# Performance work log

Hardware: AMD Instinct MI355X
Metric: run time of the kernel (lower is better)

Reference implementation:

```python
import jax, jax.numpy as jnp
import numpy as np

B, C, H, W = 4, 256, 64, 64
CK = C // 8   # 32, theta/phi channels
CV = C // 2   # 128, g channels


def setup_inputs() -> dict:
    key = jax.random.key(0)
    ks = jax.random.split(key, 10)
    s = lambda fan: 1.0 / np.sqrt(fan)
    inp = {
        "x": jax.random.normal(ks[0], (B, C, H, W), dtype=jnp.float32),
        "theta_w": jax.random.normal(ks[1], (CK, C), dtype=jnp.float32) * s(C),
        "theta_b": jax.random.normal(ks[2], (CK,), dtype=jnp.float32) * 0.01,
        "phi_w": jax.random.normal(ks[3], (CK, C), dtype=jnp.float32) * s(C),
        "phi_b": jax.random.normal(ks[4], (CK,), dtype=jnp.float32) * 0.01,
        "g_w": jax.random.normal(ks[5], (CV, C), dtype=jnp.float32) * s(C),
        "g_b": jax.random.normal(ks[6], (CV,), dtype=jnp.float32) * 0.01,
        "o_w": jax.random.normal(ks[7], (C, CV), dtype=jnp.float32) * s(CV),
        "o_b": jax.random.normal(ks[8], (C,), dtype=jnp.float32) * 0.01,
        "gamma": jax.random.normal(ks[9], (1,), dtype=jnp.float32) * 0.1,
    }
    return inp


def reference(x, theta_w, theta_b, phi_w, phi_b, g_w, g_b, o_w, o_b, gamma):
    b, c, h, w = x.shape
    n = h * w
    xf = x.reshape(b, c, n)  # [B, C, N]
    # 1x1 convs == per-pixel linear projections
    theta = jnp.einsum('oc,bcn->bon', theta_w, xf) + theta_b[None, :, None]  # [B, CK, N]
    phi = jnp.einsum('oc,bcn->bon', phi_w, xf) + phi_b[None, :, None]        # [B, CK, N]
    g = jnp.einsum('oc,bcn->bon', g_w, xf) + g_b[None, :, None]              # [B, CV, N]
    # scores[b, i, j] = theta_i . phi_j ; softmax over dim=1 (query axis i) as in torch code
    scores = jnp.einsum('bci,bcj->bij', theta, phi)  # [B, N, N]
    attention = jax.nn.softmax(scores, axis=1)
    # o_pre = bmm(g, attention^T): o_pre[b, c, i] = sum_j g[b, c, j] * attention[b, i, j]
    o_pre = jnp.einsum('bcj,bij->bci', g, attention)  # [B, CV, N]
    o = jnp.einsum('oc,bcn->bon', o_w, o_pre) + o_b[None, :, None]  # [B, C, N]
    out = (gamma[0] * o + xf).reshape(b, c, h, w)
    return out
```

## Files before the change

kernel.cpp:

```cpp
#include <hip/hip_runtime.h>
#include <math.h>

#define B_  4
#define C_  256
#define N_  4096
#define CK_ 32
#define CV_ 128

typedef __attribute__((ext_vector_type(8))) short short8;
typedef __attribute__((ext_vector_type(4))) float f32x4;
typedef unsigned short u16;
typedef unsigned int   u32;

static constexpr float LOG2E = 1.4426950408889634f;

static __device__ __forceinline__ u16 f2bf(float f) {
    u32 u = __float_as_uint(f);
    u = (u + 0x7FFFu + ((u >> 16) & 1u)) >> 16;
    return (u16)u;
}
static __device__ __forceinline__ float bf2f(u16 h) {
    return __uint_as_float(((u32)h) << 16);
}

static __device__ __forceinline__ float fexp2(float x) {
#if __has_builtin(__builtin_amdgcn_exp2f)
    return __builtin_amdgcn_exp2f(x);
#else
    float r; asm("v_exp_f32 %0, %1\n\ts_nop 0" : "=v"(r) : "v"(x)); return r;
#endif
}
static __device__ __forceinline__ float frcp(float x) {
#if __has_builtin(__builtin_amdgcn_rcpf)
    return __builtin_amdgcn_rcpf(x);
#else
    float r; asm("v_rcp_f32 %0, %1\n\ts_nop 0" : "=v"(r) : "v"(x)); return r;
#endif
}
static __device__ __forceinline__ u32 cvt_pk_bf16(float a, float b) {
    u32 r; asm("v_cvt_pk_bf16_f32 %0, %1, %2" : "=v"(r) : "v"(a), "v"(b));
    return r;
}

__global__ __launch_bounds__(256) void prep_kernel(
    const float* __restrict__ x, u16* __restrict__ xT16,
    const float* __restrict__ theta_w, const float* __restrict__ phi_w,
    const float* __restrict__ g_w,     const float* __restrict__ o_w,
    u16* __restrict__ W16, u16* __restrict__ ow16)
{
    if (blockIdx.x >= N_ / 64) {
        const int base = (((blockIdx.x - N_ / 64) * 16 + blockIdx.y * 4 + blockIdx.z) * 256
                          + threadIdx.x) * 4;
        #pragma unroll
        for (int e0 = 0; e0 < 4; ++e0) {
            const int e = base + e0;
            if (e < 8192)        W16[e] = f2bf(theta_w[e] * LOG2E);
            else if (e < 16384)  W16[e] = f2bf(phi_w[e - 8192]);
            else if (e < 49152)  W16[e] = f2bf(g_w[e - 16384]);
            else                 ow16[e - 49152] = f2bf(o_w[e - 49152]);
        }
        return;
    }

    const int b = blockIdx.z, c0 = blockIdx.y * 64, n0 = blockIdx.x * 64;
    const int t = threadIdx.x;
    __shared__ float tile[64][65];

    const int cr = t >> 4, nc = (t & 15) * 4;
    #pragma unroll
    for (int it = 0; it < 4; ++it) {
        const float4 v = *(const float4*)(x + (size_t)(b * C_ + c0 + cr + it * 16) * N_ + n0 + nc);
        tile[cr + it * 16][nc + 0] = v.x; tile[cr + it * 16][nc + 1] = v.y;
        tile[cr + it * 16][nc + 2] = v.z; tile[cr + it * 16][nc + 3] = v.w;
    }
    __syncthreads();
    const int n = t >> 2, cg = (t & 3) * 16;
    union { u16 us[16]; uint4 u4[2]; } pk;
    #pragma unroll
    for (int e = 0; e < 16; ++e) pk.us[e] = f2bf(tile[cg + e][n]);
    uint4* dst = (uint4*)(xT16 + (size_t)(b * N_ + n0 + n) * C_ + c0 + cg);
    dst[0] = pk.u4[0]; dst[1] = pk.u4[1];
}

__global__ __launch_bounds__(256) void proj_mfma_kernel(
    const u16* __restrict__ xT16, const u16* __restrict__ W16,
    const float* __restrict__ theta_b, const float* __restrict__ phi_b,
    const float* __restrict__ g_b,
    u16* __restrict__ theta_t, u16* __restrict__ phi_t, u16* __restrict__ g2)
{
    const int b = blockIdx.y, n0 = blockIdx.x * 64;
    const int w = threadIdx.x >> 6, lane = threadIdx.x & 63;
    const int lr = lane & 15, q = lane >> 4;
    const f32x4 zf = {0.f, 0.f, 0.f, 0.f};

    const u16* xrow = xT16 + (size_t)(b * N_ + n0 + w * 16 + lr) * C_;
    f32x4 acc[4];
    #pragma unroll
    for (int nt = 0; nt < 4; ++nt) acc[nt] = zf;
    for (int ks = 0; ks < 8; ++ks) {
        const short8 aX = *(const short8*)(xrow + ks * 32 + q * 8);
        #pragma unroll
        for (int nt = 0; nt < 4; ++nt) {
            const short8 bW = *(const short8*)(W16 + (size_t)(nt * 16 + lr) * C_ + ks * 32 + q * 8);
            acc[nt] = __builtin_amdgcn_mfma_f32_16x16x32_bf16(aX, bW, acc[nt], 0, 0, 0);
        }
    }
    #pragma unroll
    for (int nt = 0; nt < 4; ++nt) {
        const int o = nt * 16 + lr;
        #pragma unroll
        for (int reg = 0; reg < 4; ++reg) {
            const int n = n0 + w * 16 + q * 4 + reg;
            if (nt < 2)
                theta_t[(size_t)(b * N_ + n) * CK_ + o] = f2bf(acc[nt][reg] + theta_b[o] * LOG2E);
            else
                phi_t[(size_t)(b * N_ + n) * CK_ + (o - 32)] = f2bf(acc[nt][reg] + phi_b[o - 32]);
        }
    }

    #pragma unroll
    for (int mp = 0; mp < 2; ++mp) {
        const int ctile = w * 2 + mp;
        const int crow = ctile * 16;
        f32x4 ag[4];
        #pragma unroll
        for (int nt = 0; nt < 4; ++nt) ag[nt] = zf;
        for (int ks = 0; ks < 8; ++ks) {
            const short8 aW = *(const short8*)(W16 + (size_t)(64 + crow + lr) * C_ + ks * 32 + q * 8);
            #pragma unroll
            for (int nt = 0; nt < 4; ++nt) {
                const short8 bX = *(const short8*)(xT16 + (size_t)(b * N_ + n0 + nt * 16 + lr) * C_ + ks * 32 + q * 8);
                ag[nt] = __builtin_amdgcn_mfma_f32_16x16x32_bf16(aW, bX, ag[nt], 0, 0, 0);
            }
        }
        #pragma unroll
        for (int nt = 0; nt < 4; ++nt) {
            const int jchunk = (n0 >> 5) + (nt >> 1);
            const int lhi = (nt & 1) * 2 + (lr >> 3);
            #pragma unroll
            for (int reg = 0; reg < 4; ++reg) {
                const int c = crow + q * 4 + reg;
                const int lane2 = (q * 4 + reg) + 16 * lhi;
                g2[((size_t)(b * 8 + ctile) * 128 + jchunk) * 512 + lane2 * 8 + (lr & 7)]
                    = f2bf(ag[nt][reg] + g_b[c]);
            }
        }
    }
}

__global__ __launch_bounds__(256) void colstats_kernel(
    const u16* __restrict__ theta_t, const u16* __restrict__ phi_t,
    float* __restrict__ Z)
{
    const int b  = blockIdx.z;
    const int j0 = blockIdx.x * 32;
    const int istart = blockIdx.y * (N_ / 4);
    const int tid = threadIdx.x;
    const int wave = tid >> 6, lane = tid & 63;
    const int lr = lane & 15, q = lane >> 4;

    const int jW = j0 + (wave & 1) * 16;
    const short8 bF = *(const short8*)(phi_t + (size_t)(b * N_ + jW + lr) * CK_ + q * 8);

    const u16* thp = theta_t + (size_t)b * N_ * CK_;
    const f32x4 zero = {0.f, 0.f, 0.f, 0.f};
    float zacc = 0.f;
    for (int it = istart + (wave >> 1) * 16; it < istart + N_ / 4; it += 32) {
        const short8 aF = *(const short8*)(thp + (size_t)(it + lr) * CK_ + q * 8);
        f32x4 S = __builtin_amdgcn_mfma_f32_16x16x32_bf16(aF, bF, zero, 0, 0, 0);
        zacc += fexp2(S[0]) + fexp2(S[1]) + fexp2(S[2]) + fexp2(S[3]);
    }
    zacc += __shfl_xor(zacc, 16);
    zacc += __shfl_xor(zacc, 32);
    if (lane < 16) atomicAdd(&Z[(size_t)b * N_ + jW + lr], zacc);
}

__global__ __launch_bounds__(256) void gscale_kernel(
    u16* __restrict__ g2, const float* __restrict__ Z)
{
    const size_t idx = ((size_t)blockIdx.x * 256 + threadIdx.x) * 8;
    const int b = (int)(idx >> 19);
    const int j = (int)(((idx >> 9) & 127) * 32 + ((idx >> 7) & 3) * 8);
    uint4 raw = *(const uint4*)(g2 + idx);
    const float4 z0 = *(const float4*)(Z + (size_t)b * N_ + j);
    const float4 z1 = *(const float4*)(Z + (size_t)b * N_ + j + 4);
    const float zz[8] = {z0.x, z0.y, z0.z, z0.w, z1.x, z1.y, z1.z, z1.w};
    u16* pr = (u16*)&raw;
    union { u16 us[8]; uint4 u4; } pk;
    #pragma unroll
    for (int k = 0; k < 8; ++k) pk.us[k] = f2bf(bf2f(pr[k]) * frcp(zz[k]));
    *(uint4*)(g2 + idx) = pk.u4;
}

__global__ __launch_bounds__(256, 1) void opre_kernel(
    const u16* __restrict__ theta_t, const u16* __restrict__ phi_t,
    const u16* __restrict__ g2,
    float* __restrict__ o_p0, float* __restrict__ o_p1, u16* __restrict__ opb)
{
    const int bx = blockIdx.x;
    const int igg = bx & 7, ch = (bx >> 3) & 3, jq = (bx >> 5) & 3, b = bx >> 7;
    const int w = threadIdx.x >> 6, lane = threadIdx.x & 63;
    const int lr = lane & 15, q = lane >> 4;
    const int i0 = (igg * 4 + w) * 128;
    const f32x4 zf = {0.f, 0.f, 0.f, 0.f};

    short8 bT[8];
    #pragma unroll
    for (int it = 0; it < 8; ++it)
        bT[it] = *(const short8*)(theta_t + (size_t)(b * N_ + i0 + it * 16 + lr) * CK_ + q * 8);

    const int ja = (lr >> 2) * 8 + (lr & 3);
    const int jstart = jq * (N_ / 4);
    const u16* pA = phi_t + ((size_t)(b * N_) + jstart + ja) * CK_ + q * 8;
    const u16* pG = g2 + ((size_t)(b * 8 + ch * 2) * 128 + jq * 32) * 512 + lane * 8;

    f32x4 acc[8][2];
    #pragma unroll
    for (int it = 0; it < 8; ++it) { acc[it][0] = zf; acc[it][1] = zf; }

    short8 A0a = *(const short8*)(pA);
    short8 A1a = *(const short8*)(pA + 4 * CK_);
    short8 G0a = *(const short8*)(pG);
    short8 G1a = *(const short8*)(pG + 128 * 512);
    short8 A0b = *(const short8*)(pA + 32 * CK_);
    short8 A1b = *(const short8*)(pA + 36 * CK_);
    short8 G0b = *(const short8*)(pG + 512);
    short8 G1b = *(const short8*)(pG + 128 * 512 + 512);

#define OPRE_CHUNK(K, A0r, A1r, G0r, G1r)                                          \
    {                                                                               \
        const short8 cA0 = A0r, cA1 = A1r, cG0 = G0r, cG1 = G1r;                    \
        const int kn = ((K) + 2) & 31;                                              \
        A0r = *(const short8*)(pA + (size_t)kn * (32 * CK_));                       \
        A1r = *(const short8*)(pA + (size_t)kn * (32 * CK_) + 4 * CK_);             \
        G0r = *(const short8*)(pG + kn * 512);                                      \
        G1r = *(const short8*)(pG + 128 * 512 + kn * 512);                          \
        _Pragma("unroll")                                                           \
        for (int it = 0; it < 8; ++it) {                                            \
            const f32x4 Sa = __builtin_amdgcn_mfma_f32_16x16x32_bf16(cA0, bT[it], zf, 0, 0, 0); \
            const f32x4 Sb = __builtin_amdgcn_mfma_f32_16x16x32_bf16(cA1, bT[it], zf, 0, 0, 0); \
            union { u32 u[4]; short8 s8; } ef;                                      \
            ef.u[0] = cvt_pk_bf16(fexp2(Sa[0]), fexp2(Sa[1]));                      \
            ef.u[1] = cvt_pk_bf16(fexp2(Sa[2]), fexp2(Sa[3]));                      \
            ef.u[2] = cvt_pk_bf16(fexp2(Sb[0]), fexp2(Sb[1]));                      \
            ef.u[3] = cvt_pk_bf16(fexp2(Sb[2]), fexp2(Sb[3]));                      \
            acc[it][0] = __builtin_amdgcn_mfma_f32_16x16x32_bf16(ef.s8, cG0, acc[it][0], 0, 0, 0); \
            acc[it][1] = __builtin_amdgcn_mfma_f32_16x16x32_bf16(ef.s8, cG1, acc[it][1], 0, 0, 0); \
        }                                                                           \
    }

    for (int k = 0; k < 32; k += 2) {
        OPRE_CHUNK(k,     A0a, A1a, G0a, G1a)
        OPRE_CHUNK(k + 1, A0b, A1b, G0b, G1b)
    }
#undef OPRE_CHUNK

    if (jq < 2) {
        float* op = (jq ? o_p1 : o_p0);
        #pragma unroll
        for (int it = 0; it < 8; ++it) {
            const size_t tb = ((size_t)(b * 256 + (i0 >> 4) + it) * 4 + ch) * 512;
            #pragma unroll
            for (int ct = 0; ct < 2; ++ct) {
                #pragma unroll
                for (int reg = 0; reg < 4; ++reg) {
                    const int lane2 = (q * 4 + reg) + 16 * (ct * 2 + (lr >> 3));
                    op[tb + lane2 * 8 + (lr & 7)] = acc[it][ct][reg];
                }
            }
        }
    } else {
        u16* ob = opb + (size_t)(jq - 2) * ((size_t)B_ * N_ * CV_);
        #pragma unroll
        for (int it = 0; it < 8; ++it) {
            const size_t tb = ((size_t)(b * 256 + (i0 >> 4) + it) * 4 + ch) * 512;
            #pragma unroll
            for (int ct = 0; ct < 2; ++ct) {
                #pragma unroll
                for (int reg = 0; reg < 4; ++reg) {
                    const int lane2 = (q * 4 + reg) + 16 * (ct * 2 + (lr >> 3));
                    ob[tb + lane2 * 8 + (lr & 7)] = f2bf(acc[it][ct][reg]);
                }
            }
        }
    }
}

__global__ __launch_bounds__(256) void final_mfma_kernel(
    const float* __restrict__ o_p0, const float* __restrict__ o_p1,
    const u16* __restrict__ opb,
    const u16* __restrict__ ow16, const float* __restrict__ o_b,
    const float* __restrict__ gamma, const float* __restrict__ x,
    float* __restrict__ out)
{
    const int b = blockIdx.y, n0 = blockIdx.x * 32;
    const int w = threadIdx.x >> 6, lane = threadIdx.x & 63;
    const int lr = lane & 15, q = lane >> 4;
    const f32x4 zf = {0.f, 0.f, 0.f, 0.f};
    const size_t QS = (size_t)B_ * N_ * CV_;

    f32x4 acc[4][2];
    #pragma unroll
    for (int mt = 0; mt < 4; ++mt)
        #pragma unroll
        for (int nt = 0; nt < 2; ++nt) acc[mt][nt] = zf;

    for (int ks = 0; ks < 4; ++ks) {
        short8 bP[2];
        #pragma unroll
        for (int nt = 0; nt < 2; ++nt) {
            const size_t base = (((size_t)(b * 256 + (n0 >> 4) + nt) * 4 + ks) * 64 + lane) * 8;
            const float4 a0 = *(const float4*)(o_p0 + base);
            const float4 a1 = *(const float4*)(o_p0 + base + 4);
            const float4 c0 = *(const float4*)(o_p1 + base);
            const float4 c1 = *(const float4*)(o_p1 + base + 4);
            union { u16 us[8]; uint4 u4; } w2, w3;
            w2.u4 = *(const uint4*)(opb + base);
            w3.u4 = *(const uint4*)(opb + QS + base);
            float s[8] = {a0.x + c0.x, a0.y + c0.y, a0.z + c0.z, a0.w + c0.w,
                          a1.x + c1.x, a1.y + c1.y, a1.z + c1.z, a1.w + c1.w};
            #pragma unroll
            for (int e = 0; e < 8; ++e)
                s[e] += bf2f(w2.us[e]) + bf2f(w3.us[e]);
            union { u32 u[4]; short8 s8; } pk;
            pk.u[0] = cvt_pk_bf16(s[0], s[1]);
            pk.u[1] = cvt_pk_bf16(s[2], s[3]);
            pk.u[2] = cvt_pk_bf16(s[4], s[5]);
            pk.u[3] = cvt_pk_bf16(s[6], s[7]);
            bP[nt] = pk.s8;
        }
        #pragma unroll
        for (int mt = 0; mt < 4; ++mt) {
            const short8 aW = *(const short8*)(ow16 + (size_t)((w * 4 + mt) * 16 + lr) * CV_ + ks * 32 + q * 8);
            #pragma unroll
            for (int nt = 0; nt < 2; ++nt)
                acc[mt][nt] = __builtin_amdgcn_mfma_f32_16x16x32_bf16(aW, bP[nt], acc[mt][nt], 0, 0, 0);
        }
    }

    const float gm = gamma[0];
    #pragma unroll
    for (int mt = 0; mt < 4; ++mt) {
        #pragma unroll
        for (int nt = 0; nt < 2; ++nt) {
            #pragma unroll
            for (int reg = 0; reg < 4; ++reg) {
                const int oc = (w * 4 + mt) * 16 + q * 4 + reg;
                const int n = n0 + nt * 16 + lr;
                const size_t off = (size_t)(b * C_ + oc) * N_ + n;
                out[off] = x[off] + gm * (acc[mt][nt][reg] + o_b[oc]);
            }
        }
    }
}

extern "C" void kernel_launch(void* const* d_in, const int* in_sizes, int n_in,
                              void* d_out, int out_size, void* d_ws, size_t ws_size,
                              hipStream_t stream)
{
    const float* x       = (const float*)d_in[0];
    const float* theta_w = (const float*)d_in[1];
    const float* theta_b = (const float*)d_in[2];
    const float* phi_w   = (const float*)d_in[3];
    const float* phi_b   = (const float*)d_in[4];
    const float* g_w     = (const float*)d_in[5];
    const float* g_b     = (const float*)d_in[6];
    const float* o_w     = (const float*)d_in[7];
    const float* o_b     = (const float*)d_in[8];
    const float* gamma   = (const float*)d_in[9];
    float* out = (float*)d_out;

    u16* xT16    = (u16*)d_ws;
    u16* W16     = xT16 + (size_t)B_ * N_ * C_;
    u16* ow16    = W16 + 192 * C_;
    u16* theta_t = ow16 + C_ * CV_;
    u16* phi_t   = theta_t + (size_t)B_ * N_ * CK_;
    u16* g2      = phi_t + (size_t)B_ * N_ * CK_;
    float* Z     = (float*)(g2 + (size_t)B_ * CV_ * N_);
    float* o_p0  = Z + (size_t)B_ * N_;
    float* o_p1  = o_p0 + (size_t)B_ * N_ * CV_;
    u16* opb     = xT16;

    hipMemsetAsync(Z, 0, (size_t)B_ * N_ * sizeof(float), stream);

    prep_kernel<<<dim3(N_ / 64 + 5, C_ / 64, B_), 256, 0, stream>>>(
        x, xT16, theta_w, phi_w, g_w, o_w, W16, ow16);
    proj_mfma_kernel<<<dim3(N_ / 64, B_), 256, 0, stream>>>(
        xT16, W16, theta_b, phi_b, g_b, theta_t, phi_t, g2);
    colstats_kernel<<<dim3(N_ / 32, 4, B_), 256, 0, stream>>>(theta_t, phi_t, Z);
    gscale_kernel<<<dim3((B_ * CV_ * N_) / 2048), 256, 0, stream>>>(g2, Z);
    opre_kernel<<<dim3(512), 256, 0, stream>>>(theta_t, phi_t, g2, o_p0, o_p1, opb);
    final_mfma_kernel<<<dim3(N_ / 32, B_), 256, 0, stream>>>(
        o_p0, o_p1, opb, ow16, o_b, gamma, x, out);
}
```

Baseline: 193.7 us.

## Share exp-score tiles across channel waves through LDS in opre kernel

Before, each block handled one 32-channel slice of g, and its four waves covered different query rows. Every channel slice therefore recomputed the same theta·phi score MFMAs and exp2 values, four times over. Now a block owns 128 query rows and its four waves split the channels. Each wave computes exp scores for two 16-row tiles and writes them to a double-buffered LDS array, and all waves read all eight tiles for their PV MFMAs. This cuts score MFMAs and transcendental work by a factor of four, at the cost of a __syncthreads per chunk and extra LDS traffic.

```diff
diff --git a/kernel.cpp b/kernel.cpp
--- a/kernel.cpp
+++ b/kernel.cpp
@@ -198,21 +198,21 @@
     float* __restrict__ o_p0, float* __restrict__ o_p1, u16* __restrict__ opb)
 {
     const int bx = blockIdx.x;
-    const int igg = bx & 7, ch = (bx >> 3) & 3, jq = (bx >> 5) & 3, b = bx >> 7;
+    const int igg = bx & 31, jq = (bx >> 5) & 3, b = bx >> 7;
     const int w = threadIdx.x >> 6, lane = threadIdx.x & 63;
     const int lr = lane & 15, q = lane >> 4;
-    const int i0 = (igg * 4 + w) * 128;
+    const int i0 = igg * 128;
     const f32x4 zf = {0.f, 0.f, 0.f, 0.f};
 
-    short8 bT[8];
-    #pragma unroll
-    for (int it = 0; it < 8; ++it)
-        bT[it] = *(const short8*)(theta_t + (size_t)(b * N_ + i0 + it * 16 + lr) * CK_ + q * 8);
+    __shared__ u16 El[2][8 * 512];
+
+    const short8 bT0 = *(const short8*)(theta_t + (size_t)(b * N_ + i0 + (2 * w) * 16 + lr) * CK_ + q * 8);
+    const short8 bT1 = *(const short8*)(theta_t + (size_t)(b * N_ + i0 + (2 * w + 1) * 16 + lr) * CK_ + q * 8);
 
     const int ja = (lr >> 2) * 8 + (lr & 3);
     const int jstart = jq * (N_ / 4);
     const u16* pA = phi_t + ((size_t)(b * N_) + jstart + ja) * CK_ + q * 8;
-    const u16* pG = g2 + ((size_t)(b * 8 + ch * 2) * 128 + jq * 32) * 512 + lane * 8;
+    const u16* pG = g2 + ((size_t)(b * 8 + w * 2) * 128 + jq * 32) * 512 + lane * 8;
 
     f32x4 acc[8][2];
     #pragma unroll
@@ -227,7 +227,11 @@
     short8 G0b = *(const short8*)(pG + 512);
     short8 G1b = *(const short8*)(pG + 128 * 512 + 512);
 
-#define OPRE_CHUNK(K, A0r, A1r, G0r, G1r)                                          \
+    u16* const myE0 = &El[0][(2 * w) * 512 + lane * 8];
+    u16* const myE1 = &El[0][(2 * w + 1) * 512 + lane * 8];
+    const int bufstep = 8 * 512;
+
+#define OPRE_CHUNK(K, BUF, A0r, A1r, G0r, G1r)                                     \
     {                                                                               \
         const short8 cA0 = A0r, cA1 = A1r, cG0 = G0r, cG1 = G1r;                    \
         const int kn = ((K) + 2) & 31;                                              \
@@ -235,23 +239,34 @@
         A1r = *(const short8*)(pA + (size_t)kn * (32 * CK_) + 4 * CK_);             \
         G0r = *(const short8*)(pG + kn * 512);                                      \
         G1r = *(const short8*)(pG + 128 * 512 + kn * 512);                          \
+                                                 \
+        const f32x4 Sa0 = __builtin_amdgcn_mfma_f32_16x16x32_bf16(cA0, bT0, zf, 0, 0, 0); \
+        const f32x4 Sb0 = __builtin_amdgcn_mfma_f32_16x16x32_bf16(cA1, bT0, zf, 0, 0, 0); \
+        const f32x4 Sa1 = __builtin_amdgcn_mfma_f32_16x16x32_bf16(cA0, bT1, zf, 0, 0, 0); \
+        const f32x4 Sb1 = __builtin_amdgcn_mfma_f32_16x16x32_bf16(cA1, bT1, zf, 0, 0, 0); \
+        union { u32 u[4]; short8 s8; } e0, e1;                                      \
+        e0.u[0] = cvt_pk_bf16(fexp2(Sa0[0]), fexp2(Sa0[1]));                        \
+        e0.u[1] = cvt_pk_bf16(fexp2(Sa0[2]), fexp2(Sa0[3]));                        \
+        e0.u[2] = cvt_pk_bf16(fexp2(Sb0[0]), fexp2(Sb0[1]));                        \
+        e0.u[3] = cvt_pk_bf16(fexp2(Sb0[2]), fexp2(Sb0[3]));                        \
+        e1.u[0] = cvt_pk_bf16(fexp2(Sa1[0]), fexp2(Sa1[1]));                        \
+        e1.u[1] = cvt_pk_bf16(fexp2(Sa1[2]), fexp2(Sa1[3]));                        \
+        e1.u[2] = cvt_pk_bf16(fexp2(Sb1[0]), fexp2(Sb1[1]));                        \
+        e1.u[3] = cvt_pk_bf16(fexp2(Sb1[2]), fexp2(Sb1[3]));                        \
+        *(short8*)(myE0 + (BUF) * bufstep) = e0.s8;                                 \
+        *(short8*)(myE1 + (BUF) * bufstep) = e1.s8;                                 \
+        __syncthreads();                                                            \
         _Pragma("unroll")                                                           \
         for (int it = 0; it < 8; ++it) {                                            \
-            const f32x4 Sa = __builtin_amdgcn_mfma_f32_16x16x32_bf16(cA0, bT[it], zf, 0, 0, 0); \
-            const f32x4 Sb = __builtin_amdgcn_mfma_f32_16x16x32_bf16(cA1, bT[it], zf, 0, 0, 0); \
-            union { u32 u[4]; short8 s8; } ef;                                      \
-            ef.u[0] = cvt_pk_bf16(fexp2(Sa[0]), fexp2(Sa[1]));                      \
-            ef.u[1] = cvt_pk_bf16(fexp2(Sa[2]), fexp2(Sa[3]));                      \
-            ef.u[2] = cvt_pk_bf16(fexp2(Sb[0]), fexp2(Sb[1]));                      \
-            ef.u[3] = cvt_pk_bf16(fexp2(Sb[2]), fexp2(Sb[3]));                      \
-            acc[it][0] = __builtin_amdgcn_mfma_f32_16x16x32_bf16(ef.s8, cG0, acc[it][0], 0, 0, 0); \
-            acc[it][1] = __builtin_amdgcn_mfma_f32_16x16x32_bf16(ef.s8, cG1, acc[it][1], 0, 0, 0); \
+            const short8 eF = *(const short8*)(&El[BUF][it * 512 + lane * 8]);      \
+            acc[it][0] = __builtin_amdgcn_mfma_f32_16x16x32_bf16(eF, cG0, acc[it][0], 0, 0, 0); \
+            acc[it][1] = __builtin_amdgcn_mfma_f32_16x16x32_bf16(eF, cG1, acc[it][1], 0, 0, 0); \
         }                                                                           \
     }
 
     for (int k = 0; k < 32; k += 2) {
-        OPRE_CHUNK(k,     A0a, A1a, G0a, G1a)
-        OPRE_CHUNK(k + 1, A0b, A1b, G0b, G1b)
+        OPRE_CHUNK(k,     0, A0a, A1a, G0a, G1a)
+        OPRE_CHUNK(k + 1, 1, A0b, A1b, G0b, G1b)
     }
 #undef OPRE_CHUNK
 
@@ -259,7 +274,7 @@
         float* op = (jq ? o_p1 : o_p0);
         #pragma unroll
         for (int it = 0; it < 8; ++it) {
-            const size_t tb = ((size_t)(b * 256 + (i0 >> 4) + it) * 4 + ch) * 512;
+            const size_t tb = ((size_t)(b * 256 + (i0 >> 4) + it) * 4 + w) * 512;
             #pragma unroll
             for (int ct = 0; ct < 2; ++ct) {
                 #pragma unroll
@@ -273,7 +288,7 @@
         u16* ob = opb + (size_t)(jq - 2) * ((size_t)B_ * N_ * CV_);
         #pragma unroll
         for (int it = 0; it < 8; ++it) {
-            const size_t tb = ((size_t)(b * 256 + (i0 >> 4) + it) * 4 + ch) * 512;
+            const size_t tb = ((size_t)(b * 256 + (i0 >> 4) + it) * 4 + w) * 512;
             #pragma unroll
             for (int ct = 0; ct < 2; ++ct) {
                 #pragma unroll
```

Result: faster. 177.0 us (-8.6%).
